# Kernel optimization log

Measured on AMD Instinct MI355X. Metric: run time of the kernel, lower is better.

The kernel has to match this reference:

```python
import jax, jax.numpy as jnp
import numpy as np

D = 1024
H = 8
K = 6
TEMP = 0.1
LN_EPS = 1e-5


def _ln(x, g, b):
    m = jnp.mean(x, axis=-1, keepdims=True)
    v = jnp.mean((x - m) ** 2, axis=-1, keepdims=True)
    return (x - m) / jnp.sqrt(v + LN_EPS) * g + b


def setup_inputs() -> dict:
    key = jax.random.key(0)
    ks = jax.random.split(key, 8)
    B, T = 8, 4096
    s = 0.02
    inp = {
        'video_features': jax.random.normal(ks[0], (B, T, D), jnp.float32),
        'query_embedding': jax.random.normal(ks[1], (B, D), jnp.float32),
        'mu_w1': jax.random.normal(ks[2], (D, D), jnp.float32) * s,
        'mu_b1': jnp.zeros((D,), jnp.float32),
        'mu_g': jnp.ones((D,), jnp.float32),
        'mu_be': jnp.zeros((D,), jnp.float32),
        'mu_w2': jax.random.normal(ks[3], (D, D), jnp.float32) * s,
        'mu_b2': jnp.zeros((D,), jnp.float32),
        'sg_w1': jax.random.normal(ks[4], (D, D), jnp.float32) * s,
        'sg_b1': jnp.zeros((D,), jnp.float32),
        'sg_g': jnp.ones((D,), jnp.float32),
        'sg_be': jnp.zeros((D,), jnp.float32),
        'sg_w2': jax.random.normal(ks[5], (D, D), jnp.float32) * s,
        'sg_b2': jnp.zeros((D,), jnp.float32),
        'in_w': jax.random.normal(ks[6], (3 * D, D), jnp.float32) * s,
        'in_b': jnp.zeros((3 * D,), jnp.float32),
        'out_w': jax.random.normal(ks[7], (D, D), jnp.float32) * s,
        'out_b': jnp.zeros((D,), jnp.float32),
    }
    return inp


def reference(video_features, query_embedding, mu_w1, mu_b1, mu_g, mu_be, mu_w2, mu_b2,
              sg_w1, sg_b1, sg_g, sg_be, sg_w2, sg_b2, in_w, in_b, out_w, out_b):
    B, T, _ = video_features.shape
    dh = D // H

    # mu / sigma estimators (Linear -> LN -> ReLU -> Linear [-> Softplus])
    mu_q = jax.nn.relu(_ln(query_embedding @ mu_w1.T + mu_b1, mu_g, mu_be)) @ mu_w2.T + mu_b2  # [B,D]
    sigma_q = jax.nn.softplus(
        jax.nn.relu(_ln(query_embedding @ sg_w1.T + sg_b1, sg_g, sg_be)) @ sg_w2.T + sg_b2) + 1e-6

    # Mahalanobis (diagonal) distances [B,T]
    centered = video_features - mu_q[:, None, :]
    dist = jnp.sum(centered ** 2 / sigma_q[:, None, :], axis=-1)

    # distance weights around the (torch lower) median
    med = jnp.sort(dist, axis=1)[:, (T - 1) // 2][:, None]
    dist_w = jnp.exp(-jnp.abs(dist - med) / TEMP)  # [B,T]

    # single-query multihead attention (torch MHA, averaged attn weights)
    wq, wk, wv = in_w[:D], in_w[D:2 * D], in_w[2 * D:]
    bq, bk, bv = in_b[:D], in_b[D:2 * D], in_b[2 * D:]
    q = (mu_q @ wq.T + bq).reshape(B, H, dh)                  # [B,H,dh]
    k = (video_features @ wk.T + bk).reshape(B, T, H, dh)     # [B,T,H,dh]
    scores = jnp.einsum('bhd,bthd->bht', q, k) / jnp.sqrt(jnp.asarray(dh, q.dtype))
    attn = jax.nn.softmax(scores, axis=-1)                    # [B,H,T]
    attn_w = jnp.mean(attn, axis=1)                           # [B,T] head-averaged

    combined = dist_w * attn_w  # [B,T]

    # greedy diverse top-k (farthest-point style), vectorized over batch
    ar = jnp.arange(T)
    idx0 = jnp.argmax(combined, axis=1)                       # [B]
    sel_mask = ar[None, :] == idx0[:, None]
    min_d = jnp.abs(ar[None, :] - idx0[:, None]).astype(combined.dtype)
    picks = [idx0]
    for _ in range(K - 1):
        score = jnp.where(sel_mask, -jnp.inf, min_d * combined)
        nxt = jnp.argmax(score, axis=1)
        picks.append(nxt)
        sel_mask = sel_mask | (ar[None, :] == nxt[:, None])
        min_d = jnp.minimum(min_d, jnp.abs(ar[None, :] - nxt[:, None]).astype(combined.dtype))
    indices = jnp.stack(picks, axis=1)  # [B,K]

    rep = jnp.take_along_axis(video_features, indices[:, :, None], axis=1)  # [B,K,D]

    # NTLBG loss
    rep_dist = jnp.take_along_axis(dist, indices, axis=1)  # [B,K]
    target = jnp.sort(rep_dist, axis=1)[:, (K - 1) // 2][:, None]
    ellipsoid = jnp.mean((rep_dist - target) ** 2)
    centered_rep = rep - mu_q[:, None, :]
    consistency = jnp.mean(jnp.sum(centered_rep ** 2 / sigma_q[:, None, :], axis=-1))
    sim = jnp.einsum('bkd,bjd->bkj', rep, rep)
    tri = jnp.triu(jnp.ones((K, K), rep.dtype), k=1)
    diversity = jnp.mean((sim * tri) ** 2)
    loss = ellipsoid + 0.1 * consistency + 0.05 * diversity

    return rep, indices, combined, dist, mu_q, sigma_q, loss
```

## Files before the change

### kernel.cpp

```cpp
#include <hip/hip_runtime.h>
#include <math.h>

#define BD   8
#define TT   4096
#define DD   1024
#define HH   8
#define KK   6
#define OFF_REP   0
#define OFF_IDX   49152
#define OFF_COMB  49200
#define OFF_DIST  81968
#define OFF_MU    114736
#define OFF_SG    122928
#define OFF_LOSS  131120
#define WS_X1     0
#define WS_H      16384
#define WS_Q      32768
#define WS_P      40960
#define WS_SUMS   106496
#define WS_ISIG   106560
#define WS_ES     114752

#define INV_SQRT_DH 0.08838834764831845f

__device__ __forceinline__ float softplus_f(float x) {
  return fmaxf(x, 0.0f) + log1pf(expf(-fabsf(x)));
}

__device__ __forceinline__ void gemv_rows_core(const float* __restrict__ in,
                                               const float* __restrict__ W,
                                               int row, float (*s_in)[DD], float acc[8]) {
  int tid = threadIdx.x;
  const float4* in4 = (const float4*)in;
  float4* s4 = (float4*)&s_in[0][0];
  for (int i = tid; i < 2048; i += 256) s4[i] = in4[i];
  __syncthreads();
  int lane = tid & 63;
  const float4* wr4 = (const float4*)(W + (size_t)row * DD);
#pragma unroll
  for (int b = 0; b < 8; ++b) acc[b] = 0.0f;
#pragma unroll
  for (int i = 0; i < 4; ++i) {
    int d4 = i * 64 + lane;
    float4 w4 = wr4[d4];
#pragma unroll
    for (int b = 0; b < 8; ++b) {
      float4 q4 = ((const float4*)&s_in[b][0])[d4];
      acc[b] += w4.x * q4.x + w4.y * q4.y + w4.z * q4.z + w4.w * q4.w;
    }
  }
#pragma unroll
  for (int off = 32; off; off >>= 1)
#pragma unroll
    for (int b = 0; b < 8; ++b) acc[b] += __shfl_xor(acc[b], off, 64);
}

__global__ __launch_bounds__(256) void k_gemv_pre(const float* __restrict__ qe,
    const float* __restrict__ W0, const float* __restrict__ W1,
    const float* __restrict__ b0, const float* __restrict__ b1, float* __restrict__ x1) {
  __shared__ float s_in[8][DD];
  int path = blockIdx.x >> 8;
  int row = (blockIdx.x & 255) * 4 + (threadIdx.x >> 6);
  const float* W = path ? W1 : W0;
  const float* bb = path ? b1 : b0;
  float acc[8];
  gemv_rows_core(qe, W, row, s_in, acc);
  if ((threadIdx.x & 63) == 0) {
    float bv = bb[row];
#pragma unroll
    for (int b = 0; b < 8; ++b) x1[path * 8192 + b * DD + row] = acc[b] + bv;
  }
}

__global__ __launch_bounds__(256) void k_ln(const float* __restrict__ x1,
    const float* __restrict__ g0, const float* __restrict__ be0,
    const float* __restrict__ g1, const float* __restrict__ be1, float* __restrict__ h) {
  int path = blockIdx.x >> 3, b = blockIdx.x & 7;
  const float4* x4 = (const float4*)(x1 + path * 8192 + b * DD);
  const float4* g4 = (const float4*)(path ? g1 : g0);
  const float4* be4 = (const float4*)(path ? be1 : be0);
  int tid = threadIdx.x, wave = tid >> 6, lane = tid & 63;
  __shared__ float ws1[4], ws2[4];
  float4 v = x4[tid];
  float s = v.x + v.y + v.z + v.w;
  float s2 = v.x * v.x + v.y * v.y + v.z * v.z + v.w * v.w;
#pragma unroll
  for (int off = 32; off; off >>= 1) {
    s += __shfl_xor(s, off, 64);
    s2 += __shfl_xor(s2, off, 64);
  }
  if (lane == 0) { ws1[wave] = s; ws2[wave] = s2; }
  __syncthreads();
  s = ws1[0] + ws1[1] + ws1[2] + ws1[3];
  s2 = ws2[0] + ws2[1] + ws2[2] + ws2[3];
  float mean = s * (1.0f / 1024.0f);
  float var = s2 * (1.0f / 1024.0f) - mean * mean;
  float inv = 1.0f / sqrtf(var + 1e-5f);
  float4 g = g4[tid], be = be4[tid], o;
  o.x = fmaxf((v.x - mean) * inv * g.x + be.x, 0.0f);
  o.y = fmaxf((v.y - mean) * inv * g.y + be.y, 0.0f);
  o.z = fmaxf((v.z - mean) * inv * g.z + be.z, 0.0f);
  o.w = fmaxf((v.w - mean) * inv * g.w + be.w, 0.0f);
  ((float4*)(h + path * 8192 + b * DD))[tid] = o;
}

__global__ __launch_bounds__(256) void k_gemv_mid(const float* __restrict__ h,
    const float* __restrict__ W0, const float* __restrict__ W1,
    const float* __restrict__ b0, const float* __restrict__ b1,
    float* __restrict__ mu_out, float* __restrict__ sg_out, float* __restrict__ isig) {
  __shared__ float s_in[8][DD];
  int path = blockIdx.x >> 8;
  int row = (blockIdx.x & 255) * 4 + (threadIdx.x >> 6);
  const float* W = path ? W1 : W0;
  const float* bb = path ? b1 : b0;
  float acc[8];
  gemv_rows_core(h + path * 8192, W, row, s_in, acc);
  if ((threadIdx.x & 63) == 0) {
    float bv = bb[row];
#pragma unroll
    for (int b = 0; b < 8; ++b) {
      float v = acc[b] + bv;
      if (path == 0) {
        mu_out[b * DD + row] = v;
      } else {
        float sp = softplus_f(v) + 1e-6f;
        sg_out[b * DD + row] = sp;
        isig[b * DD + row] = 1.0f / sp;
      }
    }
  }
}

__global__ __launch_bounds__(256) void k_gemv_q(const float* __restrict__ mu_q,
    const float* __restrict__ in_w, const float* __restrict__ in_b, float* __restrict__ q) {
  __shared__ float s_in[8][DD];
  int row = blockIdx.x * 4 + (threadIdx.x >> 6);
  float acc[8];
  gemv_rows_core(mu_q, in_w, row, s_in, acc);
  if ((threadIdx.x & 63) == 0) {
    float bv = in_b[row];
#pragma unroll
    for (int b = 0; b < 8; ++b) q[b * DD + row] = acc[b] + bv;
  }
}

__global__ __launch_bounds__(256) void k_p(const float* __restrict__ q,
    const float* __restrict__ in_w, float* __restrict__ p,
    float* __restrict__ sums, float* __restrict__ loss_out) {
  if (blockIdx.x == 0) {
    if (threadIdx.x < 64) sums[threadIdx.x] = 0.0f;
    else if (threadIdx.x == 64) loss_out[0] = 0.0f;
  }
  int hh = blockIdx.x >> 2;
  int j0 = (blockIdx.x & 3) * 256;
  __shared__ float qh[8][128];
  for (int i = threadIdx.x; i < 1024; i += 256) {
    int b = i >> 7, r = i & 127;
    qh[b][r] = q[b * DD + hh * 128 + r];
  }
  __syncthreads();
  const float* wbase = in_w + (size_t)(DD + hh * 128) * DD + j0 + threadIdx.x;
  float acc[8];
#pragma unroll
  for (int b = 0; b < 8; ++b) acc[b] = 0.0f;
  for (int r = 0; r < 128; ++r) {
    float w = wbase[(size_t)r * DD];
#pragma unroll
    for (int b = 0; b < 8; ++b) acc[b] += qh[b][r] * w;
  }
#pragma unroll
  for (int b = 0; b < 8; ++b) p[(b * HH + hh) * DD + j0 + threadIdx.x] = acc[b] * INV_SQRT_DH;
}

__global__ __launch_bounds__(256, 4) void k_main(const float* __restrict__ video,
    const float* __restrict__ mu_q, const float* __restrict__ isig,
    const float* __restrict__ p,
    float* __restrict__ dist_out, float* __restrict__ es, float* __restrict__ sums) {
  __shared__ float s_mu[DD];
  __shared__ float s_is[DD];
  __shared__ float s_p[HH][DD];
  __shared__ float s_esum[HH];
  int b = blockIdx.x >> 8;
  int chunk = blockIdx.x & 255;
  int tid = threadIdx.x;
  int wave = tid >> 6, lane = tid & 63;
  float4* s_mu4 = (float4*)s_mu;
  float4* s_is4 = (float4*)s_is;
  float4* s_p4 = (float4*)&s_p[0][0];
  s_mu4[tid] = ((const float4*)(mu_q + b * DD))[tid];
  s_is4[tid] = ((const float4*)(isig + b * DD))[tid];
  const float4* pg4 = (const float4*)(p + b * HH * DD);
  for (int i = tid; i < 2048; i += 256) s_p4[i] = pg4[i];
  if (tid < HH) s_esum[tid] = 0.0f;
  __syncthreads();

  int t0 = chunk * 16 + wave * 4;
  const float4* v4 = (const float4*)(video + ((size_t)(b * TT + t0)) * DD);
  double dacc[4] = {0.0, 0.0, 0.0, 0.0};
  float sacc[4][8];
#pragma unroll
  for (int t = 0; t < 4; ++t)
#pragma unroll
    for (int hh = 0; hh < 8; ++hh) sacc[t][hh] = 0.0f;

#pragma unroll 2
  for (int i = 0; i < 4; ++i) {
    int d4 = i * 64 + lane;
    float4 vv0 = v4[0 * 256 + d4];
    float4 vv1 = v4[1 * 256 + d4];
    float4 vv2 = v4[2 * 256 + d4];
    float4 vv3 = v4[3 * 256 + d4];
    {
      float4 mu4 = s_mu4[d4];
      float4 is4 = s_is4[d4];
      float dx, dy, dz, dw, e;
      dx = vv0.x - mu4.x; dy = vv0.y - mu4.y; dz = vv0.z - mu4.z; dw = vv0.w - mu4.w;
      e = dx * dx * is4.x + dy * dy * is4.y + dz * dz * is4.z + dw * dw * is4.w;
      dacc[0] += (double)e;
      dx = vv1.x - mu4.x; dy = vv1.y - mu4.y; dz = vv1.z - mu4.z; dw = vv1.w - mu4.w;
      e = dx * dx * is4.x + dy * dy * is4.y + dz * dz * is4.z + dw * dw * is4.w;
      dacc[1] += (double)e;
      dx = vv2.x - mu4.x; dy = vv2.y - mu4.y; dz = vv2.z - mu4.z; dw = vv2.w - mu4.w;
      e = dx * dx * is4.x + dy * dy * is4.y + dz * dz * is4.z + dw * dw * is4.w;
      dacc[2] += (double)e;
      dx = vv3.x - mu4.x; dy = vv3.y - mu4.y; dz = vv3.z - mu4.z; dw = vv3.w - mu4.w;
      e = dx * dx * is4.x + dy * dy * is4.y + dz * dz * is4.z + dw * dw * is4.w;
      dacc[3] += (double)e;
    }
#pragma unroll
    for (int hh = 0; hh < 8; ++hh) {
      float4 pp = ((const float4*)&s_p[hh][0])[d4];
      sacc[0][hh] += pp.x * vv0.x + pp.y * vv0.y + pp.z * vv0.z + pp.w * vv0.w;
      sacc[1][hh] += pp.x * vv1.x + pp.y * vv1.y + pp.z * vv1.z + pp.w * vv1.w;
      sacc[2][hh] += pp.x * vv2.x + pp.y * vv2.y + pp.z * vv2.z + pp.w * vv2.w;
      sacc[3][hh] += pp.x * vv3.x + pp.y * vv3.y + pp.z * vv3.z + pp.w * vv3.w;
    }
  }
#pragma unroll
  for (int off = 32; off; off >>= 1) {
#pragma unroll
    for (int t = 0; t < 4; ++t) {
      dacc[t] += __shfl_xor(dacc[t], off, 64);
#pragma unroll
      for (int hh = 0; hh < 8; ++hh) sacc[t][hh] += __shfl_xor(sacc[t][hh], off, 64);
    }
  }
  if (lane < 4) {
    int t = lane;
    int tt = t0 + t;
    dist_out[b * TT + tt] = (float)dacc[t];
#pragma unroll
    for (int hh = 0; hh < 8; ++hh) {
      float ev = expf(sacc[t][hh]);
      es[(size_t)(b * HH + hh) * TT + tt] = ev;
      atomicAdd(&s_esum[hh], ev);
    }
  }
  __syncthreads();
  if (tid < HH) atomicAdd(&sums[b * HH + tid], s_esum[tid]);
}

__global__ __launch_bounds__(1024) void k_epilogue(const float* __restrict__ es,
    const float* __restrict__ sums,
    const float* __restrict__ dist, const float* __restrict__ video,
    float* __restrict__ comb_out, float* __restrict__ idx_out,
    float* __restrict__ rep, float* __restrict__ loss_out) {
  int b = blockIdx.x;
  int tid = threadIdx.x;
  int wave = tid >> 6, lane = tid & 63;
  __shared__ float s_dist[TT];
  __shared__ float s_hs[HH];
  __shared__ unsigned whist[16][256];
  __shared__ unsigned wsum[4];
  __shared__ unsigned s_sel;
  __shared__ int s_kk;
  __shared__ float wv[16];
  __shared__ int wi[16];
  __shared__ int s_pick;
  __shared__ float wdiv[16];
  __shared__ float repb[KK * DD];

  if (tid < HH) s_hs[tid] = 1.0f / sums[b * HH + tid];
  __syncthreads();

  float4 d4 = ((const float4*)(dist + b * TT))[tid];
  ((float4*)s_dist)[tid] = d4;
  float4 aw = make_float4(0.f, 0.f, 0.f, 0.f);
#pragma unroll
  for (int h = 0; h < HH; ++h) {
    float4 e4 = ((const float4*)(es + ((size_t)(b * HH + h)) * TT))[tid];
    float is = s_hs[h];
    aw.x += e4.x * is;
    aw.y += e4.y * is;
    aw.z += e4.z * is;
    aw.w += e4.w * is;
  }
  aw.x *= 0.125f; aw.y *= 0.125f; aw.z *= 0.125f; aw.w *= 0.125f;
  uint4 keys;
  keys.x = __float_as_uint(d4.x);
  keys.y = __float_as_uint(d4.y);
  keys.z = __float_as_uint(d4.z);
  keys.w = __float_as_uint(d4.w);

  unsigned prefix = 0;
  int kk = (TT - 1) / 2;
  for (int pass = 0; pass < 4; ++pass) {
    int shift = 24 - 8 * pass;
    ((uint4*)whist)[tid] = make_uint4(0u, 0u, 0u, 0u);
    __syncthreads();
    {
      unsigned karr[4] = {keys.x, keys.y, keys.z, keys.w};
#pragma unroll
      for (int j = 0; j < 4; ++j) {
        unsigned key = karr[j];
        bool ok = (pass == 0) || ((key >> (shift + 8)) == prefix);
        if (ok) atomicAdd(&whist[wave][(key >> shift) & 255], 1u);
      }
    }
    __syncthreads();
    unsigned hcnt = 0, inc = 0;
    if (tid < 256) {
#pragma unroll
      for (int w = 0; w < 16; ++w) hcnt += whist[w][tid];
      inc = hcnt;
#pragma unroll
      for (int off = 1; off < 64; off <<= 1) {
        unsigned v = __shfl_up(inc, off, 64);
        if (lane >= off) inc += v;
      }
      if (lane == 63) wsum[wave] = inc;
    }
    __syncthreads();
    if (tid < 256) {
      unsigned base = 0;
      for (int w = 0; w < wave; ++w) base += wsum[w];
      unsigned excl = base + inc - hcnt;
      if ((int)excl <= kk && kk < (int)(excl + hcnt)) {
        s_sel = (prefix << 8) | (unsigned)tid;
        s_kk = kk - (int)excl;
      }
    }
    __syncthreads();
    prefix = s_sel;
    kk = s_kk;
    __syncthreads();
  }
  float med = __uint_as_float(prefix);

  float4 cb;
  cb.x = expf(-fabsf(d4.x - med) / 0.1f) * aw.x;
  cb.y = expf(-fabsf(d4.y - med) / 0.1f) * aw.y;
  cb.z = expf(-fabsf(d4.z - med) / 0.1f) * aw.z;
  cb.w = expf(-fabsf(d4.w - med) / 0.1f) * aw.w;
  ((float4*)(comb_out + b * TT))[tid] = cb;

  float4 md = make_float4(0.f, 0.f, 0.f, 0.f);
  int i0 = tid * 4;
  int picks[KK];
  for (int k = 0; k < KK; ++k) {
    float carr[4] = {cb.x, cb.y, cb.z, cb.w};
    float marr[4] = {md.x, md.y, md.z, md.w};
    float best = -INFINITY; int bi = 1 << 30;
#pragma unroll
    for (int j = 0; j < 4; ++j) {
      float cv = carr[j];
      float sc = (k == 0) ? cv : ((cv < 0.0f) ? -INFINITY : marr[j] * cv);
      if (sc > best) { best = sc; bi = i0 + j; }
    }
#pragma unroll
    for (int off = 32; off; off >>= 1) {
      float ov = __shfl_xor(best, off, 64);
      int oi = __shfl_xor(bi, off, 64);
      if (ov > best || (ov == best && oi < bi)) { best = ov; bi = oi; }
    }
    if (lane == 0) { wv[wave] = best; wi[wave] = bi; }
    __syncthreads();
    if (tid == 0) {
      float bb2 = wv[0]; int ii = wi[0];
#pragma unroll
      for (int w = 1; w < 16; ++w)
        if (wv[w] > bb2 || (wv[w] == bb2 && wi[w] < ii)) { bb2 = wv[w]; ii = wi[w]; }
      s_pick = ii;
    }
    __syncthreads();
    int pick = s_pick;
    picks[k] = pick;
    if ((pick >> 2) == tid) {
      int j = pick & 3;
      if (j == 0) cb.x = -1.0f; else if (j == 1) cb.y = -1.0f;
      else if (j == 2) cb.z = -1.0f; else cb.w = -1.0f;
    }
    float dn0 = fabsf((float)(i0 + 0 - pick));
    float dn1 = fabsf((float)(i0 + 1 - pick));
    float dn2 = fabsf((float)(i0 + 2 - pick));
    float dn3 = fabsf((float)(i0 + 3 - pick));
    if (k == 0) { md.x = dn0; md.y = dn1; md.z = dn2; md.w = dn3; }
    else { md.x = fminf(md.x, dn0); md.y = fminf(md.y, dn1);
           md.z = fminf(md.z, dn2); md.w = fminf(md.w, dn3); }
  }
  if (tid < KK) idx_out[b * KK + tid] = (float)picks[tid];

  float4* repb4 = (float4*)repb;
  float4* rep4 = (float4*)(rep + (size_t)b * KK * DD);
  for (int e = tid; e < KK * (DD / 4); e += 1024) {
    int k = e >> 8, dd4 = e & 255;
    const float4* vrow = (const float4*)(video + ((size_t)(b * TT + picks[k])) * DD);
    float4 v = vrow[dd4];
    rep4[(size_t)k * (DD / 4) + dd4] = v;
    repb4[e] = v;
  }
  __syncthreads();

  const int pk[15] = {0,0,0,0,0,1,1,1,1,2,2,2,3,3,4};
  const int pj[15] = {1,2,3,4,5,2,3,4,5,3,4,5,4,5,5};
  float divacc = 0.0f;
  if (wave < 15) {
    int a = pk[wave], j = pj[wave];
    float part = 0.0f;
    for (int d = lane; d < DD; d += 64) part += repb[a * DD + d] * repb[j * DD + d];
#pragma unroll
    for (int off = 32; off; off >>= 1) part += __shfl_xor(part, off, 64);
    if (lane == 0) divacc = part * part;
  }
  if (lane == 0) wdiv[wave] = (wave < 15) ? divacc : 0.0f;
  __syncthreads();

  if (tid == 0) {
    float div = 0.0f;
#pragma unroll
    for (int w = 0; w < 15; ++w) div += wdiv[w];
    float rd[KK], srt[KK];
#pragma unroll
    for (int k = 0; k < KK; ++k) { rd[k] = s_dist[picks[k]]; srt[k] = rd[k]; }
    for (int a = 1; a < KK; ++a) {
      float key = srt[a]; int b2 = a - 1;
      while (b2 >= 0 && srt[b2] > key) { srt[b2 + 1] = srt[b2]; --b2; }
      srt[b2 + 1] = key;
    }
    float target = srt[(KK - 1) / 2];
    float ell = 0.0f, cons = 0.0f;
#pragma unroll
    for (int k = 0; k < KK; ++k) { float d = rd[k] - target; ell += d * d; cons += rd[k]; }
    float partial = ell * (1.0f / 48.0f) + 0.1f * cons * (1.0f / 48.0f) + 0.05f * div * (1.0f / 288.0f);
    atomicAdd(loss_out, partial);
  }
}

extern "C" void kernel_launch(void* const* d_in, const int* in_sizes, int n_in,
                              void* d_out, int out_size, void* d_ws, size_t ws_size,
                              hipStream_t stream) {
  const float* video = (const float*)d_in[0];
  const float* qe    = (const float*)d_in[1];
  const float* mu_w1 = (const float*)d_in[2];
  const float* mu_b1 = (const float*)d_in[3];
  const float* mu_g  = (const float*)d_in[4];
  const float* mu_be = (const float*)d_in[5];
  const float* mu_w2 = (const float*)d_in[6];
  const float* mu_b2 = (const float*)d_in[7];
  const float* sg_w1 = (const float*)d_in[8];
  const float* sg_b1 = (const float*)d_in[9];
  const float* sg_g  = (const float*)d_in[10];
  const float* sg_be = (const float*)d_in[11];
  const float* sg_w2 = (const float*)d_in[12];
  const float* sg_b2 = (const float*)d_in[13];
  const float* in_w  = (const float*)d_in[14];
  const float* in_b  = (const float*)d_in[15];
  float* out = (float*)d_out;
  float* ws  = (float*)d_ws;

  k_gemv_pre<<<512, 256, 0, stream>>>(qe, mu_w1, sg_w1, mu_b1, sg_b1, ws + WS_X1);
  k_ln<<<16, 256, 0, stream>>>(ws + WS_X1, mu_g, mu_be, sg_g, sg_be, ws + WS_H);
  k_gemv_mid<<<512, 256, 0, stream>>>(ws + WS_H, mu_w2, sg_w2, mu_b2, sg_b2,
                                      out + OFF_MU, out + OFF_SG, ws + WS_ISIG);
  k_gemv_q<<<256, 256, 0, stream>>>(out + OFF_MU, in_w, in_b, ws + WS_Q);
  k_p<<<32, 256, 0, stream>>>(ws + WS_Q, in_w, ws + WS_P, ws + WS_SUMS, out + OFF_LOSS);
  k_main<<<2048, 256, 0, stream>>>(video, out + OFF_MU, ws + WS_ISIG, ws + WS_P,
                                   out + OFF_DIST, ws + WS_ES, ws + WS_SUMS);
  k_epilogue<<<8, 1024, 0, stream>>>(ws + WS_ES, ws + WS_SUMS, out + OFF_DIST, video,
                                     out + OFF_COMB, out + OFF_IDX, out + OFF_REP, out + OFF_LOSS);
}
```

Baseline: 328.3 us.

## Halve k_main grid, loop two row groups per block, preload all video loads

Each k_main block now handles 32 timesteps in two iterations instead of 16, so the grid shrinks from 2048 to 1024 blocks. The per-block shared-memory fill of mu, isig and the P matrix is amortized over twice the rows. All 16 float4 video loads per thread are issued before any compute to expose more memory-level parallelism. The launch bound drops to 3 blocks per CU to allow the extra registers, trading occupancy for per-wave load depth.

```diff
diff --git a/kernel.cpp b/kernel.cpp
--- a/kernel.cpp
+++ b/kernel.cpp
@@ -172,7 +172,7 @@
   for (int b = 0; b < 8; ++b) p[(b * HH + hh) * DD + j0 + threadIdx.x] = acc[b] * INV_SQRT_DH;
 }
 
-__global__ __launch_bounds__(256, 4) void k_main(const float* __restrict__ video,
+__global__ __launch_bounds__(256, 3) void k_main(const float* __restrict__ video,
     const float* __restrict__ mu_q, const float* __restrict__ isig,
     const float* __restrict__ p,
     float* __restrict__ dist_out, float* __restrict__ es, float* __restrict__ sums) {
@@ -180,8 +180,8 @@
   __shared__ float s_is[DD];
   __shared__ float s_p[HH][DD];
   __shared__ float s_esum[HH];
-  int b = blockIdx.x >> 8;
-  int chunk = blockIdx.x & 255;
+  int b = blockIdx.x >> 7;
+  int group = blockIdx.x & 127;
   int tid = threadIdx.x;
   int wave = tid >> 6, lane = tid & 63;
   float4* s_mu4 = (float4*)s_mu;
@@ -194,66 +194,70 @@
   if (tid < HH) s_esum[tid] = 0.0f;
   __syncthreads();
 
-  int t0 = chunk * 16 + wave * 4;
-  const float4* v4 = (const float4*)(video + ((size_t)(b * TT + t0)) * DD);
-  double dacc[4] = {0.0, 0.0, 0.0, 0.0};
-  float sacc[4][8];
-#pragma unroll
-  for (int t = 0; t < 4; ++t)
-#pragma unroll
-    for (int hh = 0; hh < 8; ++hh) sacc[t][hh] = 0.0f;
-
-#pragma unroll 2
-  for (int i = 0; i < 4; ++i) {
-    int d4 = i * 64 + lane;
-    float4 vv0 = v4[0 * 256 + d4];
-    float4 vv1 = v4[1 * 256 + d4];
-    float4 vv2 = v4[2 * 256 + d4];
-    float4 vv3 = v4[3 * 256 + d4];
-    {
+#pragma unroll 1
+  for (int tg = 0; tg < 2; ++tg) {
+    int t0 = group * 32 + tg * 16 + wave * 4;
+    const float4* v4 = (const float4*)(video + ((size_t)(b * TT + t0)) * DD);
+
+    float4 vv[4][4];
+#pragma unroll
+    for (int i = 0; i < 4; ++i) {
+      int d4 = i * 64 + lane;
+      vv[i][0] = v4[0 * 256 + d4];
+      vv[i][1] = v4[1 * 256 + d4];
+      vv[i][2] = v4[2 * 256 + d4];
+      vv[i][3] = v4[3 * 256 + d4];
+    }
+
+    double dacc[4] = {0.0, 0.0, 0.0, 0.0};
+    float sacc[4][8];
+#pragma unroll
+    for (int t = 0; t < 4; ++t)
+#pragma unroll
+      for (int hh = 0; hh < 8; ++hh) sacc[t][hh] = 0.0f;
+
+#pragma unroll
+    for (int i = 0; i < 4; ++i) {
+      int d4 = i * 64 + lane;
       float4 mu4 = s_mu4[d4];
       float4 is4 = s_is4[d4];
-      float dx, dy, dz, dw, e;
-      dx = vv0.x - mu4.x; dy = vv0.y - mu4.y; dz = vv0.z - mu4.z; dw = vv0.w - mu4.w;
-      e = dx * dx * is4.x + dy * dy * is4.y + dz * dz * is4.z + dw * dw * is4.w;
-      dacc[0] += (double)e;
-      dx = vv1.x - mu4.x; dy = vv1.y - mu4.y; dz = vv1.z - mu4.z; dw = vv1.w - mu4.w;
-      e = dx * dx * is4.x + dy * dy * is4.y + dz * dz * is4.z + dw * dw * is4.w;
-      dacc[1] += (double)e;
-      dx = vv2.x - mu4.x; dy = vv2.y - mu4.y; dz = vv2.z - mu4.z; dw = vv2.w - mu4.w;
-      e = dx * dx * is4.x + dy * dy * is4.y + dz * dz * is4.z + dw * dw * is4.w;
-      dacc[2] += (double)e;
-      dx = vv3.x - mu4.x; dy = vv3.y - mu4.y; dz = vv3.z - mu4.z; dw = vv3.w - mu4.w;
-      e = dx * dx * is4.x + dy * dy * is4.y + dz * dz * is4.z + dw * dw * is4.w;
-      dacc[3] += (double)e;
-    }
-#pragma unroll
-    for (int hh = 0; hh < 8; ++hh) {
-      float4 pp = ((const float4*)&s_p[hh][0])[d4];
-      sacc[0][hh] += pp.x * vv0.x + pp.y * vv0.y + pp.z * vv0.z + pp.w * vv0.w;
-      sacc[1][hh] += pp.x * vv1.x + pp.y * vv1.y + pp.z * vv1.z + pp.w * vv1.w;
-      sacc[2][hh] += pp.x * vv2.x + pp.y * vv2.y + pp.z * vv2.z + pp.w * vv2.w;
-      sacc[3][hh] += pp.x * vv3.x + pp.y * vv3.y + pp.z * vv3.z + pp.w * vv3.w;
-    }
-  }
-#pragma unroll
-  for (int off = 32; off; off >>= 1) {
-#pragma unroll
-    for (int t = 0; t < 4; ++t) {
-      dacc[t] += __shfl_xor(dacc[t], off, 64);
-#pragma unroll
-      for (int hh = 0; hh < 8; ++hh) sacc[t][hh] += __shfl_xor(sacc[t][hh], off, 64);
-    }
-  }
-  if (lane < 4) {
-    int t = lane;
-    int tt = t0 + t;
-    dist_out[b * TT + tt] = (float)dacc[t];
-#pragma unroll
-    for (int hh = 0; hh < 8; ++hh) {
-      float ev = expf(sacc[t][hh]);
-      es[(size_t)(b * HH + hh) * TT + tt] = ev;
-      atomicAdd(&s_esum[hh], ev);
+#pragma unroll
+      for (int t = 0; t < 4; ++t) {
+        float dx = vv[i][t].x - mu4.x;
+        float dy = vv[i][t].y - mu4.y;
+        float dz = vv[i][t].z - mu4.z;
+        float dw = vv[i][t].w - mu4.w;
+        float e = dx * dx * is4.x + dy * dy * is4.y + dz * dz * is4.z + dw * dw * is4.w;
+        dacc[t] += (double)e;
+      }
+#pragma unroll
+      for (int hh = 0; hh < 8; ++hh) {
+        float4 pp = ((const float4*)&s_p[hh][0])[d4];
+        sacc[0][hh] += pp.x * vv[i][0].x + pp.y * vv[i][0].y + pp.z * vv[i][0].z + pp.w * vv[i][0].w;
+        sacc[1][hh] += pp.x * vv[i][1].x + pp.y * vv[i][1].y + pp.z * vv[i][1].z + pp.w * vv[i][1].w;
+        sacc[2][hh] += pp.x * vv[i][2].x + pp.y * vv[i][2].y + pp.z * vv[i][2].z + pp.w * vv[i][2].w;
+        sacc[3][hh] += pp.x * vv[i][3].x + pp.y * vv[i][3].y + pp.z * vv[i][3].z + pp.w * vv[i][3].w;
+      }
+    }
+#pragma unroll
+    for (int off = 32; off; off >>= 1) {
+#pragma unroll
+      for (int t = 0; t < 4; ++t) {
+        dacc[t] += __shfl_xor(dacc[t], off, 64);
+#pragma unroll
+        for (int hh = 0; hh < 8; ++hh) sacc[t][hh] += __shfl_xor(sacc[t][hh], off, 64);
+      }
+    }
+    if (lane < 4) {
+      int t = lane;
+      int tt = t0 + t;
+      dist_out[b * TT + tt] = (float)dacc[t];
+#pragma unroll
+      for (int hh = 0; hh < 8; ++hh) {
+        float ev = expf(sacc[t][hh]);
+        es[(size_t)(b * HH + hh) * TT + tt] = ev;
+        atomicAdd(&s_esum[hh], ev);
+      }
     }
   }
   __syncthreads();
@@ -474,7 +478,7 @@
                                       out + OFF_MU, out + OFF_SG, ws + WS_ISIG);
   k_gemv_q<<<256, 256, 0, stream>>>(out + OFF_MU, in_w, in_b, ws + WS_Q);
   k_p<<<32, 256, 0, stream>>>(ws + WS_Q, in_w, ws + WS_P, ws + WS_SUMS, out + OFF_LOSS);
-  k_main<<<2048, 256, 0, stream>>>(video, out + OFF_MU, ws + WS_ISIG, ws + WS_P,
+  k_main<<<1024, 256, 0, stream>>>(video, out + OFF_MU, ws + WS_ISIG, ws + WS_P,
                                    out + OFF_DIST, ws + WS_ES, ws + WS_SUMS);
   k_epilogue<<<8, 1024, 0, stream>>>(ws + WS_ES, ws + WS_SUMS, out + OFF_DIST, video,
                                      out + OFF_COMB, out + OFF_IDX, out + OFF_REP, out + OFF_LOSS);
```

Measured after the change: 426.4 us. +29.9%, slower.
